# Optimization experiments

Hardware: AMD Instinct MI355X
Metric: run time of the kernel (lower is better)

## Reference

```python
import jax, jax.numpy as jnp
import numpy as np

B, D_MODEL, N, H = 4, 256, 2048, 4
HEAD_DIM = D_MODEL // H  # 64


def _rotate_half(x):
    # x: [..., d] with d even; pairs (x1, x2) -> (-x2, x1)
    x = x.reshape(x.shape[:-1] + (x.shape[-1] // 2, 2))
    x1, x2 = x[..., 0], x[..., 1]
    return jnp.stack((-x2, x1), axis=-1).reshape(x.shape[:-2] + (-1,))


def _apply_rope(freqs, t):
    # freqs: [2, n, d] (cos, sin); t: [b, h, n, d]
    return t * freqs[0] + _rotate_half(t) * freqs[1]


def setup_inputs() -> dict:
    key = jax.random.key(0)
    ks = jax.random.split(key, 12)
    s = 0.02
    inp = {
        "query": jax.random.normal(ks[0], (B, D_MODEL, N), jnp.float32),
        "key": jax.random.normal(ks[1], (B, D_MODEL, N), jnp.float32),
        "value": jax.random.normal(ks[2], (B, D_MODEL, N), jnp.float32),
        "encoding": jax.random.normal(ks[3], (2, N, HEAD_DIM), jnp.float32),
        "Wq": jax.random.normal(ks[4], (D_MODEL, D_MODEL), jnp.float32) * s,
        "bq": jnp.zeros((D_MODEL,), jnp.float32),
        "Wk": jax.random.normal(ks[5], (D_MODEL, D_MODEL), jnp.float32) * s,
        "bk": jnp.zeros((D_MODEL,), jnp.float32),
        "Wv": jax.random.normal(ks[6], (D_MODEL, D_MODEL), jnp.float32) * s,
        "bv": jnp.zeros((D_MODEL,), jnp.float32),
        "Wm": jax.random.normal(ks[7], (D_MODEL, D_MODEL), jnp.float32) * s,
        "bm": jnp.zeros((D_MODEL,), jnp.float32),
    }
    return inp


def _proj(W, b, x):
    # 1x1 Conv1d == channel matmul: x [b, c_in, n] -> [b, c_out, n]
    return jnp.einsum('oi,bin->bon', W, x) + b[None, :, None]


def reference(query, key, value, encoding, Wq, bq, Wk, bk, Wv, bv, Wm, bm):
    b = query.shape[0]
    # project and split channels into (head_dim, heads): [b, d, h, n]
    q = _proj(Wq, bq, query).reshape(b, HEAD_DIM, H, -1)
    k = _proj(Wk, bk, key).reshape(b, HEAD_DIM, H, -1)
    v = _proj(Wv, bv, value).reshape(b, HEAD_DIM, H, -1)
    # RoPE on [b, h, n, d] layout
    q = jnp.transpose(_apply_rope(encoding, jnp.transpose(q, (0, 2, 3, 1))), (0, 3, 1, 2))
    k = jnp.transpose(_apply_rope(encoding, jnp.transpose(k, (0, 2, 3, 1))), (0, 3, 1, 2))
    # attention: scores [b, h, n, m]
    scores = jnp.einsum('bdhn,bdhm->bhnm', q, k) / jnp.sqrt(jnp.float32(HEAD_DIM))
    prob = jax.nn.softmax(scores, axis=-1)
    x = jnp.einsum('bhnm,bdhm->bdhn', prob, v)
    x = x.reshape(b, HEAD_DIM * H, -1)
    return _proj(Wm, bm, x)
```

## Files before the change

### kernel.cpp

```cpp
#include <hip/hip_runtime.h>
#include <stdint.h>

#define NSEQ 2048

typedef __attribute__((ext_vector_type(4))) float f32x4;
typedef __attribute__((ext_vector_type(8))) short s16x8;
typedef _Float16 f16x8 __attribute__((ext_vector_type(8)));

#define OFF_XT  0u
#define OFF_PO  0u
#define OFF_M   16777216u
#define OFF_L   17301504u
#define OFF_QR  17825792u
#define OFF_KR  22020096u
#define OFF_VT  26214400u
#define OFF_W   30408704u

__device__ __forceinline__ short f2h(float f) {
  _Float16 h = (_Float16)f;
  return __builtin_bit_cast(short, h);
}
__device__ __forceinline__ float h2f(short s) {
  return (float)__builtin_bit_cast(_Float16, s);
}
__device__ __forceinline__ int swz128(int row, int slot) {
  return row * 128 + ((slot ^ (row & 7)) << 4);
}
#define MFMA(a, b, c) __builtin_amdgcn_mfma_f32_16x16x32_f16(a, b, c, 0, 0, 0)

__global__ void k_convw(const float* __restrict__ Wq, const float* __restrict__ Wk,
                        const float* __restrict__ Wv, const float* __restrict__ Wm,
                        char* __restrict__ ws) {
  int o = blockIdx.x, which = blockIdx.y, i = threadIdx.x;
  const float* src = which == 0 ? Wq : which == 1 ? Wk : which == 2 ? Wv : Wm;
  short* dst = (short*)(ws + OFF_W) + which * 65536;
  float val = (which < 3) ? src[o * 256 + i] : src[o * 256 + ((i & 63) << 2) + (i >> 6)];
  dst[o * 256 + i] = f2h(val);
}

__global__ __launch_bounds__(256) void k_trans(const float* __restrict__ q,
    const float* __restrict__ k, const float* __restrict__ v, char* __restrict__ ws) {
  int tensor = blockIdx.z >> 2, b = blockIdx.z & 3;
  const float* src = tensor == 0 ? q : (tensor == 1 ? k : v);
  short* dst = (short*)(ws + OFF_XT) + (tensor * 4 + b) * 524288;
  int n0 = blockIdx.x * 64, i0 = blockIdx.y * 64;
  __shared__ float tile[64][65];
  int t = threadIdx.x;
  int nl = t & 63, ib = (t >> 6) * 16;
#pragma unroll
  for (int r = 0; r < 16; ++r)
    tile[ib + r][nl] = src[(b * 256 + i0 + ib + r) * 2048 + n0 + nl];
  __syncthreads();
  int nr = t >> 2, ic = (t & 3) * 16;
  short tmp[16];
#pragma unroll
  for (int j = 0; j < 16; ++j) tmp[j] = f2h(tile[ic + j][nr]);
  short* dp = &dst[(n0 + nr) * 256 + i0 + ic];
  *(s16x8*)dp = *(const s16x8*)&tmp[0];
  *(s16x8*)(dp + 8) = *(const s16x8*)&tmp[8];
}

__global__ __launch_bounds__(256) void k_proj(const float* __restrict__ enc,
    const float* __restrict__ bq, const float* __restrict__ bk,
    const float* __restrict__ bv, char* __restrict__ ws) {
  int hid = blockIdx.x + 32 * (blockIdx.y + 4 * blockIdx.z);
  int fm = (hid & 7) * 192 + (hid >> 3);
  int yo = fm & 3, xn = (fm >> 2) & 31, z = fm >> 7;
  int proj = z >> 2, b = z & 3;
  const short* W = (const short*)(ws + OFF_W) + proj * 65536;
  const short* X = (const short*)(ws + OFF_XT) + (proj * 4 + b) * 524288;
  int o0 = yo * 64, n0 = xn * 64;
  __shared__ short As[64 * 64], Bs[64 * 64];
  int t = threadIdx.x, lane = t & 63, g = lane >> 4, c = lane & 15, wave = t >> 6;
  int wr = wave >> 1, wc = wave & 1;
  int row = t >> 2, seg = t & 3;
  f32x4 acc[2][2] = {};
  for (int kk = 0; kk < 4; ++kk) {
    __syncthreads();
    int koff = kk * 64;
    const short* wsrc = &W[(o0 + row) * 256 + koff];
    const short* xsrc = &X[(n0 + row) * 256 + koff];
    *(s16x8*)((char*)As + swz128(row, seg))     = *(const s16x8*)(wsrc + seg * 8);
    *(s16x8*)((char*)As + swz128(row, 4 + seg)) = *(const s16x8*)(wsrc + 32 + seg * 8);
    *(s16x8*)((char*)Bs + swz128(row, seg))     = *(const s16x8*)(xsrc + seg * 8);
    *(s16x8*)((char*)Bs + swz128(row, 4 + seg)) = *(const s16x8*)(xsrc + 32 + seg * 8);
    __syncthreads();
#pragma unroll
    for (int ks = 0; ks < 2; ++ks) {
      f16x8 af[2], bfr[2];
#pragma unroll
      for (int f = 0; f < 2; ++f) {
        af[f]  = *(const f16x8*)((char*)As + swz128(wr * 32 + f * 16 + c, ks * 4 + g));
        bfr[f] = *(const f16x8*)((char*)Bs + swz128(wc * 32 + f * 16 + c, ks * 4 + g));
      }
#pragma unroll
      for (int i = 0; i < 2; ++i)
#pragma unroll
        for (int j = 0; j < 2; ++j)
          acc[i][j] = MFMA(af[i], bfr[j], acc[i][j]);
    }
  }
  const float* bias = proj == 0 ? bq : (proj == 1 ? bk : bv);
  if (proj < 2) {
    short* dst0 = (short*)(ws + (proj == 0 ? OFF_QR : OFF_KR));
    float scale = proj == 0 ? 0.18033688f : 1.0f;
    float sgn = (g & 1) ? 1.0f : -1.0f;
#pragma unroll
    for (int i = 0; i < 2; ++i) {
      int ob = o0 + wr * 32 + i * 16 + g * 4;
      int d = ob >> 2;
#pragma unroll
      for (int j = 0; j < 2; ++j) {
        int n = n0 + wc * 32 + j * 16 + c;
        float cv = enc[n * 64 + d], sv = enc[131072 + n * 64 + d];
#pragma unroll
        for (int r = 0; r < 4; ++r) {
          float val = acc[i][j][r] + bias[ob + r];
          float par = __shfl_xor(val, 16, 64);
          float res = (val * cv + sgn * par * sv) * scale;
          dst0[((b * 4 + r) * 2048 + n) * 64 + d] = f2h(res);
        }
      }
    }
  } else {
    short* dst = (short*)(ws + OFF_VT);
#pragma unroll
    for (int i = 0; i < 2; ++i) {
      int ob = o0 + wr * 32 + i * 16 + g * 4;
      int d = ob >> 2;
#pragma unroll
      for (int j = 0; j < 2; ++j) {
        int n = n0 + wc * 32 + j * 16 + c;
#pragma unroll
        for (int r = 0; r < 4; ++r) {
          float val = acc[i][j][r] + bias[ob + r];
          dst[((b * 4 + r) * 64 + d) * 2048 + n] = f2h(val);
        }
      }
    }
  }
}

__global__ __launch_bounds__(256, 4) void k_attn(char* __restrict__ ws) {
  int bh = blockIdx.y, ms = blockIdx.z;
  int t = threadIdx.x, wave = t >> 6, lane = t & 63, g = lane >> 4, c = lane & 15;
  int nw = blockIdx.x * 64 + wave * 16;
  const short* Q = (const short*)(ws + OFF_QR) + bh * 131072;
  const short* K = (const short*)(ws + OFF_KR) + bh * 131072;
  const short* V = (const short*)(ws + OFF_VT) + bh * 131072;
  __shared__ short Ks[64 * 64], Vs[64 * 64], Ps[4][16 * 64];
  char* Pb = (char*)Ps[wave];
  f16x8 qf0 = *(const f16x8*)&Q[(nw + c) * 64 + g * 8];
  f16x8 qf1 = *(const f16x8*)&Q[(nw + c) * 64 + 32 + g * 8];
  f32x4 po[4] = {};
  float mrun = -1e30f, lrun = 0.f;
  int sr = t >> 3, sl = t & 7;
  const int mb = ms * 512;
  int bsrc = g * 16 + g * 4;

  s16x8 RA[4], RB[4];
  auto LD = [&](int m0, s16x8* R) {
    R[0] = *(const s16x8*)&K[(m0 + sr) * 64 + sl * 8];
    R[1] = *(const s16x8*)&K[(m0 + sr + 32) * 64 + sl * 8];
    R[2] = *(const s16x8*)&V[sr * 2048 + m0 + sl * 8];
    R[3] = *(const s16x8*)&V[(sr + 32) * 2048 + m0 + sl * 8];
  };
  auto ST = [&](const s16x8* R) {
    *(s16x8*)((char*)Ks + swz128(sr, sl))      = R[0];
    *(s16x8*)((char*)Ks + swz128(sr + 32, sl)) = R[1];
    *(s16x8*)((char*)Vs + swz128(sr, sl))      = R[2];
    *(s16x8*)((char*)Vs + swz128(sr + 32, sl)) = R[3];
  };
  auto COMPUTE = [&]() {
    f32x4 s[4] = {};
    __builtin_amdgcn_s_setprio(1);
#pragma unroll
    for (int fj = 0; fj < 4; ++fj) {
      f16x8 k0 = *(const f16x8*)((char*)Ks + swz128(fj * 16 + c, g));
      f16x8 k1 = *(const f16x8*)((char*)Ks + swz128(fj * 16 + c, 4 + g));
      s[fj] = MFMA(k0, qf0, s[fj]);
      s[fj] = MFMA(k1, qf1, s[fj]);
    }
    __builtin_amdgcn_s_setprio(0);
    float t0 = fmaxf(fmaxf(s[0][0], s[0][1]), fmaxf(s[0][2], s[0][3]));
    float t1 = fmaxf(fmaxf(s[1][0], s[1][1]), fmaxf(s[1][2], s[1][3]));
    float t2 = fmaxf(fmaxf(s[2][0], s[2][1]), fmaxf(s[2][2], s[2][3]));
    float t3 = fmaxf(fmaxf(s[3][0], s[3][1]), fmaxf(s[3][2], s[3][3]));
    float rmax = fmaxf(fmaxf(t0, t1), fmaxf(t2, t3));
    rmax = fmaxf(rmax, __shfl_xor(rmax, 16, 64));
    rmax = fmaxf(rmax, __shfl_xor(rmax, 32, 64));
    if (__any(rmax > mrun + 11.5f)) {
      float nm = fmaxf(mrun, rmax);
      float corr = exp2f(mrun - nm);
      mrun = nm;
      lrun *= corr;
#pragma unroll
      for (int r = 0; r < 4; ++r) {
        float corr_r = __shfl(corr, bsrc + r, 64);
#pragma unroll
        for (int fd = 0; fd < 4; ++fd) po[fd][r] *= corr_r;
      }
    }
    float p[4][4], rs = 0.f;
#pragma unroll
    for (int fj = 0; fj < 4; ++fj) {
      f32x4 pv;
#pragma unroll
      for (int r = 0; r < 4; ++r) {
        pv[r] = exp2f(s[fj][r] - mrun);
        p[fj][r] = pv[r];
      }
      rs += (pv[0] + pv[1]) + (pv[2] + pv[3]);
    }
    rs += __shfl_xor(rs, 16, 64);
    rs += __shfl_xor(rs, 32, 64);
    lrun += rs;
#pragma unroll
    for (int fj = 0; fj < 4; ++fj)
#pragma unroll
      for (int r = 0; r < 4; ++r) {
        int mm = fj * 16 + g * 4 + r;
        *(short*)(Pb + swz128(c, mm >> 3) + (mm & 7) * 2) = f2h(p[fj][r]);
      }
    asm volatile("s_waitcnt lgkmcnt(0)" ::: "memory");
    __builtin_amdgcn_sched_barrier(0);
    f16x8 pa0 = *(const f16x8*)(Pb + swz128(c, g));
    f16x8 pa1 = *(const f16x8*)(Pb + swz128(c, 4 + g));
    __builtin_amdgcn_s_setprio(1);
#pragma unroll
    for (int fd = 0; fd < 4; ++fd) {
      int dd = fd * 16 + c;
      f16x8 vb0 = *(const f16x8*)((char*)Vs + swz128(dd, g));
      f16x8 vb1 = *(const f16x8*)((char*)Vs + swz128(dd, 4 + g));
      po[fd] = MFMA(pa0, vb0, po[fd]);
      po[fd] = MFMA(pa1, vb1, po[fd]);
    }
    __builtin_amdgcn_s_setprio(0);
  };

  LD(mb, RA);
  for (int tt = 0; tt < 8; tt += 2) {
    __syncthreads();
    ST(RA);
    LD(mb + (tt + 1) * 64, RB);
    __syncthreads();
    COMPUTE();
    __syncthreads();
    ST(RB);
    if (tt + 2 < 8) LD(mb + (tt + 2) * 64, RA);
    __syncthreads();
    COMPUTE();
  }

  short* PO = (short*)(ws + OFF_PO);
  float* Mm = (float*)(ws + OFF_M);
  float* Ll = (float*)(ws + OFF_L);
  int base = (ms * 16 + bh) * 2048;
  float li[4];
#pragma unroll
  for (int r = 0; r < 4; ++r) li[r] = 1.0f / __shfl(lrun, bsrc + r, 64);
  asm volatile("s_waitcnt lgkmcnt(0)" ::: "memory");
  __builtin_amdgcn_sched_barrier(0);
#pragma unroll
  for (int fd = 0; fd < 4; ++fd) {
    int d = fd * 16 + c;
#pragma unroll
    for (int r = 0; r < 4; ++r)
      *(short*)(Pb + swz128(g * 4 + r, d >> 3) + (d & 7) * 2) = f2h(po[fd][r] * li[r]);
  }
  asm volatile("s_waitcnt lgkmcnt(0)" ::: "memory");
  __builtin_amdgcn_sched_barrier(0);
  int rr = lane >> 2, ds = (lane & 3) * 16;
  s16x8 v0 = *(const s16x8*)(Pb + swz128(rr, ds >> 3));
  s16x8 v1 = *(const s16x8*)(Pb + swz128(rr, (ds >> 3) + 1));
  *(s16x8*)&PO[(base + nw + rr) * 64 + ds]     = v0;
  *(s16x8*)&PO[(base + nw + rr) * 64 + ds + 8] = v1;
  if (g == 0) {
    Mm[base + nw + c] = mrun;
    Ll[base + nw + c] = lrun;
  }
}

__global__ __launch_bounds__(256) void k_final(const float* __restrict__ bm,
    float* __restrict__ out, char* __restrict__ ws) {
  int hid = blockIdx.x + 64 * (blockIdx.y + 4 * blockIdx.z);
  int fm = (hid & 7) * 128 + (hid >> 3);
  int yo = fm & 3, xn = (fm >> 2) & 63, b = fm >> 8;
  int o0 = yo * 64, n0 = xn * 32;
  const short* Wf = (const short*)(ws + OFF_W) + 3 * 65536;
  const short* PO = (const short*)(ws + OFF_PO);
  const float* Mm = (const float*)(ws + OFF_M);
  const float* Ll = (const float*)(ws + OFF_L);
  __shared__ short As[64 * 64], Bs[32 * 64];
  int t = threadIdx.x, lane = t & 63, g = lane >> 4, c = lane & 15, wave = t >> 6;
  int wr = wave >> 1, wc = wave & 1;
  int arow = t >> 2, aseg = t & 3;
  int brow = t >> 3, bseg = t & 7;
  f32x4 acc[2] = {};
  for (int kk = 0; kk < 4; ++kk) {
    __syncthreads();
    const short* wsrc = &Wf[(o0 + arow) * 256 + kk * 64];
    *(s16x8*)((char*)As + swz128(arow, aseg))     = *(const s16x8*)(wsrc + aseg * 8);
    *(s16x8*)((char*)As + swz128(arow, 4 + aseg)) = *(const s16x8*)(wsrc + 32 + aseg * 8);
    int bh = b * 4 + kk;
    int nr = n0 + brow;
    float m0 = Mm[(0 * 16 + bh) * 2048 + nr], l0 = Ll[(0 * 16 + bh) * 2048 + nr];
    float m1 = Mm[(1 * 16 + bh) * 2048 + nr], l1 = Ll[(1 * 16 + bh) * 2048 + nr];
    float m2 = Mm[(2 * 16 + bh) * 2048 + nr], l2 = Ll[(2 * 16 + bh) * 2048 + nr];
    float m3 = Mm[(3 * 16 + bh) * 2048 + nr], l3 = Ll[(3 * 16 + bh) * 2048 + nr];
    float M = fmaxf(fmaxf(m0, m1), fmaxf(m2, m3));
    float w0 = l0 * exp2f(m0 - M), w1 = l1 * exp2f(m1 - M);
    float w2 = l2 * exp2f(m2 - M), w3 = l3 * exp2f(m3 - M);
    float inv = 1.f / (w0 + w1 + w2 + w3);
    w0 *= inv; w1 *= inv; w2 *= inv; w3 *= inv;
    s16x8 a0 = *(const s16x8*)&PO[((0 * 16 + bh) * 2048 + nr) * 64 + bseg * 8];
    s16x8 a1 = *(const s16x8*)&PO[((1 * 16 + bh) * 2048 + nr) * 64 + bseg * 8];
    s16x8 a2 = *(const s16x8*)&PO[((2 * 16 + bh) * 2048 + nr) * 64 + bseg * 8];
    s16x8 a3 = *(const s16x8*)&PO[((3 * 16 + bh) * 2048 + nr) * 64 + bseg * 8];
    short hb[8];
#pragma unroll
    for (int j = 0; j < 8; ++j)
      hb[j] = f2h(w0 * h2f(a0[j]) + w1 * h2f(a1[j]) + w2 * h2f(a2[j]) + w3 * h2f(a3[j]));
    *(s16x8*)((char*)Bs + swz128(brow, bseg)) = *(const s16x8*)hb;
    __syncthreads();
#pragma unroll
    for (int ks = 0; ks < 2; ++ks) {
      f16x8 af[2], bfr;
#pragma unroll
      for (int f = 0; f < 2; ++f)
        af[f] = *(const f16x8*)((char*)As + swz128(wr * 32 + f * 16 + c, ks * 4 + g));
      bfr = *(const f16x8*)((char*)Bs + swz128(wc * 16 + c, ks * 4 + g));
#pragma unroll
      for (int i = 0; i < 2; ++i)
        acc[i] = MFMA(af[i], bfr, acc[i]);
    }
  }
#pragma unroll
  for (int i = 0; i < 2; ++i) {
    int ob = o0 + wr * 32 + i * 16 + g * 4;
    int n = n0 + wc * 16 + c;
#pragma unroll
    for (int r = 0; r < 4; ++r)
      out[(b * 256 + ob + r) * 2048 + n] = acc[i][r] + bm[ob + r];
  }
}

extern "C" void kernel_launch(void* const* d_in, const int* in_sizes, int n_in,
                              void* d_out, int out_size, void* d_ws, size_t ws_size,
                              hipStream_t stream) {
  (void)in_sizes; (void)n_in; (void)out_size; (void)ws_size;
  const float* q   = (const float*)d_in[0];
  const float* k   = (const float*)d_in[1];
  const float* v   = (const float*)d_in[2];
  const float* enc = (const float*)d_in[3];
  const float* Wq  = (const float*)d_in[4];
  const float* bq  = (const float*)d_in[5];
  const float* Wk  = (const float*)d_in[6];
  const float* bk  = (const float*)d_in[7];
  const float* Wv  = (const float*)d_in[8];
  const float* bv  = (const float*)d_in[9];
  const float* Wm  = (const float*)d_in[10];
  const float* bm  = (const float*)d_in[11];
  char* ws = (char*)d_ws;
  float* out = (float*)d_out;
  hipLaunchKernelGGL(k_convw, dim3(256, 4), dim3(256), 0, stream, Wq, Wk, Wv, Wm, ws);
  hipLaunchKernelGGL(k_trans, dim3(32, 4, 12), dim3(256), 0, stream, q, k, v, ws);
  hipLaunchKernelGGL(k_proj, dim3(32, 4, 12), dim3(256), 0, stream, enc, bq, bk, bv, ws);
  hipLaunchKernelGGL(k_attn, dim3(32, 16, 4), dim3(256), 0, stream, ws);
  hipLaunchKernelGGL(k_final, dim3(64, 4, 4), dim3(256), 0, stream, bm, out, ws);
}
```

Baseline: 161.9 us.

## Fuse input transpose into projection kernel and pack P stores

Removes the separate transpose/convert kernel and has the projection kernel read fp32 inputs directly, transposing and converting them to fp16 through a shared-memory tile per K step. This drops one launch and the round trip of the fp16 transposed copy through global memory. The trade-off is that each output-channel block now re-reads and re-converts the same input tile (four times across o-blocks), and an extra barrier is added per K step. In attention, the probability tile is packed with cvt_pkrtz and written as 8-byte stores instead of scalar 16-bit stores, which changes rounding to round-toward-zero.

```diff
diff --git a/kernel.cpp b/kernel.cpp
--- a/kernel.cpp
+++ b/kernel.cpp
@@ -6,8 +6,10 @@
 typedef __attribute__((ext_vector_type(4))) float f32x4;
 typedef __attribute__((ext_vector_type(8))) short s16x8;
 typedef _Float16 f16x8 __attribute__((ext_vector_type(8)));
-
-#define OFF_XT  0u
+typedef _Float16 h16x2 __attribute__((ext_vector_type(2)));
+typedef unsigned int u32;
+typedef __attribute__((ext_vector_type(2))) unsigned int u32x2;
+
 #define OFF_PO  0u
 #define OFF_M   16777216u
 #define OFF_L   17301504u
@@ -38,52 +40,42 @@
   dst[o * 256 + i] = f2h(val);
 }
 
-__global__ __launch_bounds__(256) void k_trans(const float* __restrict__ q,
-    const float* __restrict__ k, const float* __restrict__ v, char* __restrict__ ws) {
-  int tensor = blockIdx.z >> 2, b = blockIdx.z & 3;
-  const float* src = tensor == 0 ? q : (tensor == 1 ? k : v);
-  short* dst = (short*)(ws + OFF_XT) + (tensor * 4 + b) * 524288;
-  int n0 = blockIdx.x * 64, i0 = blockIdx.y * 64;
-  __shared__ float tile[64][65];
-  int t = threadIdx.x;
-  int nl = t & 63, ib = (t >> 6) * 16;
-#pragma unroll
-  for (int r = 0; r < 16; ++r)
-    tile[ib + r][nl] = src[(b * 256 + i0 + ib + r) * 2048 + n0 + nl];
-  __syncthreads();
-  int nr = t >> 2, ic = (t & 3) * 16;
-  short tmp[16];
-#pragma unroll
-  for (int j = 0; j < 16; ++j) tmp[j] = f2h(tile[ic + j][nr]);
-  short* dp = &dst[(n0 + nr) * 256 + i0 + ic];
-  *(s16x8*)dp = *(const s16x8*)&tmp[0];
-  *(s16x8*)(dp + 8) = *(const s16x8*)&tmp[8];
-}
-
-__global__ __launch_bounds__(256) void k_proj(const float* __restrict__ enc,
-    const float* __restrict__ bq, const float* __restrict__ bk,
-    const float* __restrict__ bv, char* __restrict__ ws) {
+__global__ __launch_bounds__(256) void k_proj(const float* __restrict__ q,
+    const float* __restrict__ k, const float* __restrict__ v,
+    const float* __restrict__ enc, const float* __restrict__ bq,
+    const float* __restrict__ bk, const float* __restrict__ bv, char* __restrict__ ws) {
   int hid = blockIdx.x + 32 * (blockIdx.y + 4 * blockIdx.z);
   int fm = (hid & 7) * 192 + (hid >> 3);
   int yo = fm & 3, xn = (fm >> 2) & 31, z = fm >> 7;
   int proj = z >> 2, b = z & 3;
+  const float* xs = proj == 0 ? q : (proj == 1 ? k : v);
   const short* W = (const short*)(ws + OFF_W) + proj * 65536;
-  const short* X = (const short*)(ws + OFF_XT) + (proj * 4 + b) * 524288;
   int o0 = yo * 64, n0 = xn * 64;
   __shared__ short As[64 * 64], Bs[64 * 64];
+  __shared__ float ftile[64][65];
   int t = threadIdx.x, lane = t & 63, g = lane >> 4, c = lane & 15, wave = t >> 6;
   int wr = wave >> 1, wc = wave & 1;
   int row = t >> 2, seg = t & 3;
+  int nl = t & 63, ib = (t >> 6) * 16;
   f32x4 acc[2][2] = {};
   for (int kk = 0; kk < 4; ++kk) {
-    __syncthreads();
     int koff = kk * 64;
+    __syncthreads();
     const short* wsrc = &W[(o0 + row) * 256 + koff];
-    const short* xsrc = &X[(n0 + row) * 256 + koff];
-    *(s16x8*)((char*)As + swz128(row, seg))     = *(const s16x8*)(wsrc + seg * 8);
-    *(s16x8*)((char*)As + swz128(row, 4 + seg)) = *(const s16x8*)(wsrc + 32 + seg * 8);
-    *(s16x8*)((char*)Bs + swz128(row, seg))     = *(const s16x8*)(xsrc + seg * 8);
-    *(s16x8*)((char*)Bs + swz128(row, 4 + seg)) = *(const s16x8*)(xsrc + 32 + seg * 8);
+    s16x8 wa0 = *(const s16x8*)(wsrc + seg * 8);
+    s16x8 wa1 = *(const s16x8*)(wsrc + 32 + seg * 8);
+#pragma unroll
+    for (int r = 0; r < 16; ++r)
+      ftile[ib + r][nl] = xs[(b * 256 + koff + ib + r) * 2048 + n0 + nl];
+    *(s16x8*)((char*)As + swz128(row, seg))     = wa0;
+    *(s16x8*)((char*)As + swz128(row, 4 + seg)) = wa1;
+    __syncthreads();
+    int ic = seg * 16;
+    short hb[16];
+#pragma unroll
+    for (int j = 0; j < 16; ++j) hb[j] = f2h(ftile[ic + j][row]);
+    *(s16x8*)((char*)Bs + swz128(row, ic >> 3))       = *(const s16x8*)&hb[0];
+    *(s16x8*)((char*)Bs + swz128(row, (ic >> 3) + 1)) = *(const s16x8*)&hb[8];
     __syncthreads();
 #pragma unroll
     for (int ks = 0; ks < 2; ++ks) {
@@ -216,12 +208,13 @@
     rs += __shfl_xor(rs, 32, 64);
     lrun += rs;
 #pragma unroll
-    for (int fj = 0; fj < 4; ++fj)
-#pragma unroll
-      for (int r = 0; r < 4; ++r) {
-        int mm = fj * 16 + g * 4 + r;
-        *(short*)(Pb + swz128(c, mm >> 3) + (mm & 7) * 2) = f2h(p[fj][r]);
-      }
+    for (int fj = 0; fj < 4; ++fj) {
+      u32 lo = __builtin_bit_cast(u32, __builtin_amdgcn_cvt_pkrtz(p[fj][0], p[fj][1]));
+      u32 hi = __builtin_bit_cast(u32, __builtin_amdgcn_cvt_pkrtz(p[fj][2], p[fj][3]));
+      u32x2 pk; pk[0] = lo; pk[1] = hi;
+      int slot = (fj * 16 + g * 4) >> 3;
+      *(u32x2*)(Pb + swz128(c, slot) + (g & 1) * 8) = pk;
+    }
     asm volatile("s_waitcnt lgkmcnt(0)" ::: "memory");
     __builtin_amdgcn_sched_barrier(0);
     f16x8 pa0 = *(const f16x8*)(Pb + swz128(c, g));
@@ -364,8 +357,7 @@
   char* ws = (char*)d_ws;
   float* out = (float*)d_out;
   hipLaunchKernelGGL(k_convw, dim3(256, 4), dim3(256), 0, stream, Wq, Wk, Wv, Wm, ws);
-  hipLaunchKernelGGL(k_trans, dim3(32, 4, 12), dim3(256), 0, stream, q, k, v, ws);
-  hipLaunchKernelGGL(k_proj, dim3(32, 4, 12), dim3(256), 0, stream, enc, bq, bk, bv, ws);
+  hipLaunchKernelGGL(k_proj, dim3(32, 4, 12), dim3(256), 0, stream, q, k, v, enc, bq, bk, bv, ws);
   hipLaunchKernelGGL(k_attn, dim3(32, 16, 4), dim3(256), 0, stream, ws);
   hipLaunchKernelGGL(k_final, dim3(64, 4, 4), dim3(256), 0, stream, bm, out, ws);
 }
```

Result: no change. 162.7 us (+0.4%).
